# Kernel tuning notes

Hardware: AMD Instinct MI355X
Metric: run time of the kernel (lower is better)

## Reference

```python
import jax, jax.numpy as jnp
import numpy as np


def setup_inputs() -> dict:
    key = jax.random.key(0)
    k1, k2 = jax.random.split(key)
    B, S, D = 8, 4096, 1024
    E, P = 8, 4
    x = jax.random.normal(k1, (B, S, D), dtype=jnp.float32)
    phi_kernel = jax.random.normal(k2, (D, E * P), dtype=jnp.float32) * (1.0 / np.sqrt(D))
    phi_bias = jnp.zeros((E * P,), dtype=jnp.float32)
    return {"x": x, "phi_kernel": phi_kernel, "phi_bias": phi_bias,
            "num_experts": E, "num_slots": P}


def reference(x, phi_kernel, phi_bias, num_experts, num_slots):
    B, S, D = x.shape
    E, P = num_experts, num_slots
    # phi logits: [B,S,E,P]
    phi_logits = (jnp.einsum('bsd,dk->bsk', x, phi_kernel) + phi_bias).reshape(B, S, E, P)
    # softmax over the sequence axis (each slot is a convex combo of tokens)
    phi_weights = jax.nn.softmax(phi_logits, axis=1)
    # soft slots: weighted sum over tokens -> [B,E,P,D] (fused, no [B,S,E,P,D] blowup)
    soft_slots = jnp.einsum('bsd,bsep->bepd', x, phi_weights)
    expert_inputs = soft_slots.reshape(B, E, P * D)
    expert_weights = jnp.full((B, S, E), 1.0 / E, dtype=x.dtype)
    expert_indices = jnp.broadcast_to(jnp.arange(E, dtype=jnp.int32)[None, None, :], (B, S, E))
    return (expert_weights, expert_indices, phi_weights, soft_slots, expert_inputs)
```

## Files before the change

kernel.cpp:

```cpp
#include <hip/hip_runtime.h>
#include <hip/hip_bf16.h>

#define B 8
#define S 4096
#define DD 1024
#define KK 32

typedef __attribute__((ext_vector_type(8))) short bf16x8;
typedef __attribute__((ext_vector_type(16))) float f32x16;

static __device__ __forceinline__ unsigned short f2bf(float f) {
    unsigned int u = __builtin_bit_cast(unsigned int, f);
    u += 0x7FFFu + ((u >> 16) & 1u);
    return (unsigned short)(u >> 16);
}

__global__ __launch_bounds__(256) void k0_phit(const float* __restrict__ phi,
                                               unsigned short* __restrict__ phiT) {
    __shared__ float lt[32][33];
    const int d0 = blockIdx.x * 32;
    const int tid = threadIdx.x;
#pragma unroll
    for (int i = 0; i < 4; ++i) {
        int slot = tid + i * 256;
        int d = slot >> 5, k = slot & 31;
        lt[d][k] = phi[(size_t)(d0 + d) * KK + k];
    }
    __syncthreads();
    const int k = tid >> 3, c = tid & 7, d = c * 4;
    short4 pk;
    pk.x = (short)f2bf(lt[d + 0][k]);
    pk.y = (short)f2bf(lt[d + 1][k]);
    pk.z = (short)f2bf(lt[d + 2][k]);
    pk.w = (short)f2bf(lt[d + 3][k]);
    *(short4*)(phiT + (size_t)k * DD + d0 + d) = pk;
}

__global__ __launch_bounds__(256) void k1_logits(const float* __restrict__ x,
                                                 const unsigned short* __restrict__ phiT,
                                                 const float* __restrict__ bias,
                                                 float* __restrict__ lp) {
    __shared__ __align__(16) char sm[32768 + 2 * 16384];

    const int bid = blockIdx.x;
    const int dq = bid & 1;
    const int st = (bid >> 1) & 31;
    const int b  = bid >> 6;
    const int s0 = st * 128;
    const int tid = threadIdx.x;
    const int wv = __builtin_amdgcn_readfirstlane(tid >> 6);
    const int lane = tid & 63;
    const int l31 = lane & 31;
    const int half = lane >> 5;

    {
        const uint4* pg = (const uint4*)phiT;
#pragma unroll
        for (int i = 0; i < 8; ++i) {
            int slot = tid + i * 256;
            int k = slot >> 6, blk = slot & 63;
            uint4 v = pg[(size_t)k * 128 + dq * 64 + blk];
            *(uint4*)(sm + (size_t)k * 1024 + ((blk ^ (k & 7)) << 4)) = v;
        }
    }

    f32x16 acc;
    {
        float bv = (dq == 0) ? bias[l31] : 0.f;
#pragma unroll
        for (int r = 0; r < 16; ++r) acc[r] = bv;
    }

    const float* xg = x + ((size_t)(b * S + s0)) * DD + dq * 512;

    float4 q[8];
    auto load8 = [&](int ch) {
#pragma unroll
        for (int i = 0; i < 8; ++i) {
            int slot = tid + i * 256;
            int s = slot >> 4, c4 = slot & 15;
            q[i] = *(const float4*)(xg + (size_t)s * DD + ch * 64 + c4 * 4);
        }
    };
    auto store8 = [&](char* buf) {
#pragma unroll
        for (int i = 0; i < 8; ++i) {
            int slot = tid + i * 256;
            int s = slot >> 4, c4 = slot & 15;
            short4 pk;
            pk.x = (short)f2bf(q[i].x);
            pk.y = (short)f2bf(q[i].y);
            pk.z = (short)f2bf(q[i].z);
            pk.w = (short)f2bf(q[i].w);
            *(short4*)(buf + (size_t)s * 128 + (((c4 >> 1) ^ (s & 7)) << 4) + (c4 & 1) * 8) = pk;
        }
    };

    load8(0);
    store8(sm + 32768);
    __syncthreads();

    const int srow = wv * 32 + l31;
    const int sx = srow & 7;
    const int kx = l31 & 7;

    for (int ch = 0; ch < 8; ++ch) {
        char* cur = sm + 32768 + (ch & 1) * 16384;
        char* nxt = sm + 32768 + ((ch & 1) ^ 1) * 16384;
        if (ch < 7) load8(ch + 1);
#pragma unroll
        for (int step = 0; step < 4; ++step) {
            int blk = step * 2 + half;
            bf16x8 af  = *(const bf16x8*)(cur + (size_t)srow * 128 + ((blk ^ sx) << 4));
            bf16x8 bfv = *(const bf16x8*)(sm + (size_t)l31 * 1024 + (((ch * 8 + blk) ^ kx) << 4));
            acc = __builtin_amdgcn_mfma_f32_32x32x16_bf16(af, bfv, acc, 0, 0, 0);
        }
        __syncthreads();
        if (ch < 7) store8(nxt);
        __syncthreads();
    }

    float* lt = (float*)(sm + 32768);
#pragma unroll
    for (int r = 0; r < 16; ++r) {
        int row = (r & 3) + 8 * (r >> 2) + 4 * half;
        lt[(size_t)l31 * 129 + wv * 32 + row] = acc[r];
    }
    __syncthreads();
    float* o = lp + ((size_t)(dq * B + b) * KK) * S + s0;
#pragma unroll
    for (int i = 0; i < 4; ++i) {
        int slot = tid + i * 256;
        int k = slot >> 5, s4 = slot & 31;
        float4 v;
        v.x = lt[k * 129 + s4 * 4 + 0];
        v.y = lt[k * 129 + s4 * 4 + 1];
        v.z = lt[k * 129 + s4 * 4 + 2];
        v.w = lt[k * 129 + s4 * 4 + 3];
        *(float4*)(o + (size_t)k * S + s4 * 4) = v;
    }
}

__global__ __launch_bounds__(256) void k2a_partial(const float* __restrict__ lp,
                                                   float* __restrict__ pmax,
                                                   float* __restrict__ psum) {
    const int bid = blockIdx.x;
    const int c  = bid & 7;
    const int bk = bid >> 3;
    const int tid = threadIdx.x;
    const int wave = tid >> 6, lane = tid & 63;
    const size_t base = (size_t)bk * S + c * 512;

    float v0 = lp[base + tid]       + lp[1048576 + base + tid];
    float v1 = lp[base + tid + 256] + lp[1048576 + base + tid + 256];

    float m = fmaxf(v0, v1);
#pragma unroll
    for (int off = 32; off >= 1; off >>= 1) m = fmaxf(m, __shfl_xor(m, off, 64));
    __shared__ float sm_[4], sl[4];
    if (lane == 0) sm_[wave] = m;
    __syncthreads();
    const float M = fmaxf(fmaxf(sm_[0], sm_[1]), fmaxf(sm_[2], sm_[3]));

    float l = __expf(v0 - M) + __expf(v1 - M);
#pragma unroll
    for (int off = 32; off >= 1; off >>= 1) l += __shfl_xor(l, off, 64);
    if (lane == 0) sl[wave] = l;
    __syncthreads();
    if (tid == 0) {
        pmax[bid] = M;
        psum[bid] = sl[0] + sl[1] + sl[2] + sl[3];
    }
}

__global__ __launch_bounds__(256) void k2c_norm(const float* __restrict__ lp,
                                                const float* __restrict__ pmax,
                                                const float* __restrict__ psum,
                                                unsigned short* __restrict__ wbT,
                                                float* __restrict__ pw_out) {
    __shared__ float tile[128][33];
    __shared__ float sM[32], sLinv[32];
    const int b  = blockIdx.x >> 5;
    const int sc = blockIdx.x & 31;
    const int s0 = sc * 128;
    const int tid = threadIdx.x;

    if (tid < 32) {
        const int k = tid;
        float M = -1e30f, L = 0.f;
#pragma unroll
        for (int c = 0; c < 8; ++c) {
            float mc = pmax[(b * KK + k) * 8 + c];
            float lc = psum[(b * KK + k) * 8 + c];
            float nM = fmaxf(M, mc);
            L = L * __expf(M - nM) + lc * __expf(mc - nM);
            M = nM;
        }
        sM[k] = M;
        sLinv[k] = 1.0f / L;
    }
    __syncthreads();

    const int sL = tid & 127;
    const int kh = tid >> 7;
#pragma unroll
    for (int kk = 0; kk < 16; ++kk) {
        const int k = kk * 2 + kh;
        const size_t idx = ((size_t)b * KK + k) * S + s0 + sL;
        float v = lp[idx] + lp[1048576 + idx];
        float w = __expf(v - sM[k]) * sLinv[k];
        wbT[idx] = f2bf(w);
        tile[sL][k] = w;
    }
    __syncthreads();

    float* ob = pw_out + ((size_t)b * S + s0) * KK;
#pragma unroll
    for (int i = 0; i < 4; ++i) {
        const int idx4 = tid + i * 256;
        const int sl = idx4 >> 3, kq = idx4 & 7;
        float4 v4 = make_float4(tile[sl][kq * 4 + 0], tile[sl][kq * 4 + 1],
                                tile[sl][kq * 4 + 2], tile[sl][kq * 4 + 3]);
        ((float4*)ob)[idx4] = v4;
    }
}

__global__ __launch_bounds__(256) void k3_slots(const float* __restrict__ x,
                                                const unsigned int* __restrict__ wbT32,
                                                float* __restrict__ part) {
    __shared__ __align__(16) char sm[2 * 16384 + 2 * 4096];

    const int bid = blockIdx.x;
    const int sc = bid & 7;
    const int dg = (bid >> 3) & 7;
    const int b  = bid >> 6;
    const int tid = threadIdx.x;
    const int wv = __builtin_amdgcn_readfirstlane(tid >> 6);
    const int lane = tid & 63;
    const int l31 = lane & 31;
    const int half = lane >> 5;

    const int dth = tid & 127;
    const int sh  = tid >> 7;

    const float* xg = x + ((size_t)(b * S + sc * 512)) * DD + dg * 128 + dth;
    const unsigned int* wg = wbT32 + (size_t)b * KK * (S / 2) + sc * 256;

    float q0[16], q1[16];
    unsigned int qw[4];
    auto loadc = [&](int ch) {
#pragma unroll
        for (int j = 0; j < 16; ++j) {
            int sp = sh * 16 + j;
            q0[j] = xg[(size_t)(ch * 64 + sp * 2) * DD];
            q1[j] = xg[(size_t)(ch * 64 + sp * 2 + 1) * DD];
        }
#pragma unroll
        for (int i = 0; i < 4; ++i) {
            int slot = tid + i * 256;
            int k = slot >> 5, c = slot & 31;
            qw[i] = wg[(size_t)k * (S / 2) + ch * 32 + c];
        }
    };
    auto storec = [&](char* xB, char* wB) {
#pragma unroll
        for (int j = 0; j < 16; ++j) {
            int sp = sh * 16 + j;
            unsigned int pkd = (unsigned int)f2bf(q0[j]) | ((unsigned int)f2bf(q1[j]) << 16);
            *(unsigned int*)(xB + (size_t)dth * 128 + (((sp >> 2) ^ (dth & 7)) << 4) + (sp & 3) * 4) = pkd;
        }
#pragma unroll
        for (int i = 0; i < 4; ++i) {
            int slot = tid + i * 256;
            int k = slot >> 5, c = slot & 31;
            *(unsigned int*)(wB + (size_t)k * 128 + (((c >> 2) ^ (k & 7)) << 4) + (c & 3) * 4) = qw[i];
        }
    };

    f32x16 acc;
#pragma unroll
    for (int r = 0; r < 16; ++r) acc[r] = 0.f;

    loadc(0);
    storec(sm, sm + 32768);
    __syncthreads();

    const int dloc = wv * 32 + l31;
    const int dx = dloc & 7;
    const int kx = l31 & 7;

    for (int ch = 0; ch < 8; ++ch) {
        const int cur = ch & 1;
        char* xCur = sm + cur * 16384;
        char* wCur = sm + 32768 + cur * 4096;
        char* xNxt = sm + (cur ^ 1) * 16384;
        char* wNxt = sm + 32768 + (cur ^ 1) * 4096;
        if (ch < 7) loadc(ch + 1);
#pragma unroll
        for (int step = 0; step < 4; ++step) {
            int blk = step * 2 + half;
            bf16x8 af  = *(const bf16x8*)(wCur + (size_t)l31 * 128 + ((blk ^ kx) << 4));
            bf16x8 bfv = *(const bf16x8*)(xCur + (size_t)dloc * 128 + ((blk ^ dx) << 4));
            acc = __builtin_amdgcn_mfma_f32_32x32x16_bf16(af, bfv, acc, 0, 0, 0);
        }
        __syncthreads();
        if (ch < 7) storec(xNxt, wNxt);
        __syncthreads();
    }

    float* pp = part + (((size_t)sc * B + b) * KK) * DD + dg * 128 + wv * 32 + l31;
#pragma unroll
    for (int r = 0; r < 16; ++r) {
        int k = (r & 3) + 8 * (r >> 2) + 4 * half;
        pp[(size_t)k * DD] = acc[r];
    }
}

__global__ __launch_bounds__(256) void k4_finalize(const float* __restrict__ part,
                                                   float* __restrict__ out) {
    const int idx = blockIdx.x * 256 + threadIdx.x;
    const float4* p4 = (const float4*)part;

    float4 sv = p4[idx];
#pragma unroll
    for (int c = 1; c < 8; ++c) {
        float4 t = p4[(size_t)c * 65536 + idx];
        sv.x += t.x; sv.y += t.y; sv.z += t.z; sv.w += t.w;
    }

    ((float4*)(out + 1572864))[idx] = sv;
    ((float4*)(out + 1835008))[idx] = sv;
    ((float4*)out)[idx] = make_float4(0.125f, 0.125f, 0.125f, 0.125f);
    float base = (float)((idx * 4) & 7);
    ((float4*)(out + 262144))[idx] = make_float4(base, base + 1.f, base + 2.f, base + 3.f);
}

extern "C" void kernel_launch(void* const* d_in, const int* in_sizes, int n_in,
                              void* d_out, int out_size, void* d_ws, size_t ws_size,
                              hipStream_t stream) {
    const float* x    = (const float*)d_in[0];
    const float* phi  = (const float*)d_in[1];
    const float* bias = (const float*)d_in[2];
    float* out = (float*)d_out;

    float* ws = (float*)d_ws;
    float* lp   = ws;
    float* pmax = ws + 2097152;
    float* psum = ws + 2099200;
    unsigned short* wbT  = (unsigned short*)(ws + 2101248);
    unsigned short* phiT = (unsigned short*)(ws + 2625536);
    float* part = ws + 2641920;
    float* pw_out = out + 524288;

    k0_phit<<<dim3(32), dim3(256), 0, stream>>>(phi, phiT);
    k1_logits<<<dim3(512), dim3(256), 0, stream>>>(x, phiT, bias, lp);
    k2a_partial<<<dim3(2048), dim3(256), 0, stream>>>(lp, pmax, psum);
    k2c_norm<<<dim3(256), dim3(256), 0, stream>>>(lp, pmax, psum, wbT, pw_out);
    k3_slots<<<dim3(512), dim3(256), 0, stream>>>(x, (const unsigned int*)wbT, part);
    k4_finalize<<<dim3(256), dim3(256), 0, stream>>>(part, out);
}
```

Before: 234.6 us.

## Load MFMA operands directly from global in logits and use async LDS loads in slots

```diff
diff --git a/kernel.cpp b/kernel.cpp
--- a/kernel.cpp
+++ b/kernel.cpp
@@ -13,6 +13,16 @@
     unsigned int u = __builtin_bit_cast(unsigned int, f);
     u += 0x7FFFu + ((u >> 16) & 1u);
     return (unsigned short)(u >> 16);
+}
+
+static __device__ __forceinline__ unsigned int pack2bf(float lo, float hi) {
+    return (unsigned int)f2bf(lo) | ((unsigned int)f2bf(hi) << 16);
+}
+
+static __device__ __forceinline__ void gload_lds16(const void* g, void* l) {
+    __builtin_amdgcn_global_load_lds(
+        (const __attribute__((address_space(1))) unsigned int*)g,
+        (__attribute__((address_space(3))) unsigned int*)l, 16, 0, 0);
 }
 
 __global__ __launch_bounds__(256) void k0_phit(const float* __restrict__ phi,
@@ -40,13 +50,13 @@
                                                  const unsigned short* __restrict__ phiT,
                                                  const float* __restrict__ bias,
                                                  float* __restrict__ lp) {
-    __shared__ __align__(16) char sm[32768 + 2 * 16384];
+    __shared__ __align__(16) char sm[32768];
+    __shared__ float lt[32][129];
 
     const int bid = blockIdx.x;
     const int dq = bid & 1;
     const int st = (bid >> 1) & 31;
     const int b  = bid >> 6;
-    const int s0 = st * 128;
     const int tid = threadIdx.x;
     const int wv = __builtin_amdgcn_readfirstlane(tid >> 6);
     const int lane = tid & 63;
@@ -70,73 +80,43 @@
 #pragma unroll
         for (int r = 0; r < 16; ++r) acc[r] = bv;
     }
-
-    const float* xg = x + ((size_t)(b * S + s0)) * DD + dq * 512;
-
-    float4 q[8];
-    auto load8 = [&](int ch) {
-#pragma unroll
-        for (int i = 0; i < 8; ++i) {
-            int slot = tid + i * 256;
-            int s = slot >> 4, c4 = slot & 15;
-            q[i] = *(const float4*)(xg + (size_t)s * DD + ch * 64 + c4 * 4);
-        }
-    };
-    auto store8 = [&](char* buf) {
-#pragma unroll
-        for (int i = 0; i < 8; ++i) {
-            int slot = tid + i * 256;
-            int s = slot >> 4, c4 = slot & 15;
-            short4 pk;
-            pk.x = (short)f2bf(q[i].x);
-            pk.y = (short)f2bf(q[i].y);
-            pk.z = (short)f2bf(q[i].z);
-            pk.w = (short)f2bf(q[i].w);
-            *(short4*)(buf + (size_t)s * 128 + (((c4 >> 1) ^ (s & 7)) << 4) + (c4 & 1) * 8) = pk;
-        }
-    };
-
-    load8(0);
-    store8(sm + 32768);
-    __syncthreads();
-
-    const int srow = wv * 32 + l31;
-    const int sx = srow & 7;
+    __syncthreads();
+
+    const float* xg = x + ((size_t)(b * S + st * 128 + wv * 32 + l31)) * DD
+                        + dq * 512 + half * 8;
     const int kx = l31 & 7;
-
-    for (int ch = 0; ch < 8; ++ch) {
-        char* cur = sm + 32768 + (ch & 1) * 16384;
-        char* nxt = sm + 32768 + ((ch & 1) ^ 1) * 16384;
-        if (ch < 7) load8(ch + 1);
-#pragma unroll
-        for (int step = 0; step < 4; ++step) {
-            int blk = step * 2 + half;
-            bf16x8 af  = *(const bf16x8*)(cur + (size_t)srow * 128 + ((blk ^ sx) << 4));
-            bf16x8 bfv = *(const bf16x8*)(sm + (size_t)l31 * 1024 + (((ch * 8 + blk) ^ kx) << 4));
-            acc = __builtin_amdgcn_mfma_f32_32x32x16_bf16(af, bfv, acc, 0, 0, 0);
-        }
-        __syncthreads();
-        if (ch < 7) store8(nxt);
-        __syncthreads();
-    }
-
-    float* lt = (float*)(sm + 32768);
+    const char* brow = sm + (size_t)l31 * 1024;
+
+#pragma unroll 8
+    for (int ch = 0; ch < 32; ++ch) {
+        float4 a0 = *(const float4*)(xg + ch * 16);
+        float4 a1 = *(const float4*)(xg + ch * 16 + 4);
+        unsigned int p0 = pack2bf(a0.x, a0.y);
+        unsigned int p1 = pack2bf(a0.z, a0.w);
+        unsigned int p2 = pack2bf(a1.x, a1.y);
+        unsigned int p3 = pack2bf(a1.z, a1.w);
+        uint4 pv = make_uint4(p0, p1, p2, p3);
+        bf16x8 af = __builtin_bit_cast(bf16x8, pv);
+        bf16x8 bfv = *(const bf16x8*)(brow + (((ch * 2 + half) ^ kx) << 4));
+        acc = __builtin_amdgcn_mfma_f32_32x32x16_bf16(af, bfv, acc, 0, 0, 0);
+    }
+
 #pragma unroll
     for (int r = 0; r < 16; ++r) {
         int row = (r & 3) + 8 * (r >> 2) + 4 * half;
-        lt[(size_t)l31 * 129 + wv * 32 + row] = acc[r];
-    }
-    __syncthreads();
-    float* o = lp + ((size_t)(dq * B + b) * KK) * S + s0;
+        lt[l31][wv * 32 + row] = acc[r];
+    }
+    __syncthreads();
+    float* o = lp + ((size_t)(dq * B + b) * KK) * S + st * 128;
 #pragma unroll
     for (int i = 0; i < 4; ++i) {
         int slot = tid + i * 256;
         int k = slot >> 5, s4 = slot & 31;
         float4 v;
-        v.x = lt[k * 129 + s4 * 4 + 0];
-        v.y = lt[k * 129 + s4 * 4 + 1];
-        v.z = lt[k * 129 + s4 * 4 + 2];
-        v.w = lt[k * 129 + s4 * 4 + 3];
+        v.x = lt[k][s4 * 4 + 0];
+        v.y = lt[k][s4 * 4 + 1];
+        v.z = lt[k][s4 * 4 + 2];
+        v.w = lt[k][s4 * 4 + 3];
         *(float4*)(o + (size_t)k * S + s4 * 4) = v;
     }
 }
@@ -226,9 +206,9 @@
 }
 
 __global__ __launch_bounds__(256) void k3_slots(const float* __restrict__ x,
-                                                const unsigned int* __restrict__ wbT32,
+                                                const unsigned short* __restrict__ wbT,
                                                 float* __restrict__ part) {
-    __shared__ __align__(16) char sm[2 * 16384 + 2 * 4096];
+    __shared__ __align__(16) char sm[2 * 32768 + 2 * 4096];
 
     const int bid = blockIdx.x;
     const int sc = bid & 7;
@@ -240,75 +220,55 @@
     const int l31 = lane & 31;
     const int half = lane >> 5;
 
-    const int dth = tid & 127;
-    const int sh  = tid >> 7;
-
-    const float* xg = x + ((size_t)(b * S + sc * 512)) * DD + dg * 128 + dth;
-    const unsigned int* wg = wbT32 + (size_t)b * KK * (S / 2) + sc * 256;
-
-    float q0[16], q1[16];
-    unsigned int qw[4];
-    auto loadc = [&](int ch) {
-#pragma unroll
-        for (int j = 0; j < 16; ++j) {
-            int sp = sh * 16 + j;
-            q0[j] = xg[(size_t)(ch * 64 + sp * 2) * DD];
-            q1[j] = xg[(size_t)(ch * 64 + sp * 2 + 1) * DD];
-        }
-#pragma unroll
-        for (int i = 0; i < 4; ++i) {
-            int slot = tid + i * 256;
-            int k = slot >> 5, c = slot & 31;
-            qw[i] = wg[(size_t)k * (S / 2) + ch * 32 + c];
-        }
+    const char* xsrc = (const char*)(x + ((size_t)(b * S + sc * 512 + wv * 16 + half)) * DD
+                                       + dg * 128 + l31 * 4);
+    const int wk = wv * 8 + (lane >> 3);
+    const char* wsrc = (const char*)wbT + ((size_t)(b * KK + wk) * S + sc * 512) * 2
+                                        + (((lane & 7) ^ (wk & 7)) << 4);
+
+    char* const xb0 = sm;
+    char* const wb0 = sm + 65536;
+
+    auto stage = [&](int ch, int buf) {
+        char* xb = xb0 + buf * 32768 + wv * (16 * 512);
+        const char* xs = xsrc + (size_t)ch * (64 * DD * 4);
+#pragma unroll
+        for (int t = 0; t < 8; ++t)
+            gload_lds16(xs + (size_t)t * (2 * DD * 4), xb + t * 1024);
+        gload_lds16(wsrc + (size_t)ch * 128, wb0 + buf * 4096 + wv * 1024);
     };
-    auto storec = [&](char* xB, char* wB) {
-#pragma unroll
-        for (int j = 0; j < 16; ++j) {
-            int sp = sh * 16 + j;
-            unsigned int pkd = (unsigned int)f2bf(q0[j]) | ((unsigned int)f2bf(q1[j]) << 16);
-            *(unsigned int*)(xB + (size_t)dth * 128 + (((sp >> 2) ^ (dth & 7)) << 4) + (sp & 3) * 4) = pkd;
-        }
-#pragma unroll
-        for (int i = 0; i < 4; ++i) {
-            int slot = tid + i * 256;
-            int k = slot >> 5, c = slot & 31;
-            *(unsigned int*)(wB + (size_t)k * 128 + (((c >> 2) ^ (k & 7)) << 4) + (c & 3) * 4) = qw[i];
-        }
-    };
 
     f32x16 acc;
 #pragma unroll
     for (int r = 0; r < 16; ++r) acc[r] = 0.f;
 
-    loadc(0);
-    storec(sm, sm + 32768);
-    __syncthreads();
-
-    const int dloc = wv * 32 + l31;
-    const int dx = dloc & 7;
+    stage(0, 0);
+    __syncthreads();
+
+    const int col = wv * 32 + l31;
     const int kx = l31 & 7;
 
     for (int ch = 0; ch < 8; ++ch) {
         const int cur = ch & 1;
-        char* xCur = sm + cur * 16384;
-        char* wCur = sm + 32768 + cur * 4096;
-        char* xNxt = sm + (cur ^ 1) * 16384;
-        char* wNxt = sm + 32768 + (cur ^ 1) * 4096;
-        if (ch < 7) loadc(ch + 1);
+        if (ch < 7) stage(ch + 1, cur ^ 1);
+        const float* xr = (const float*)(xb0 + cur * 32768);
+        const char* wr = wb0 + cur * 4096 + (size_t)l31 * 128;
 #pragma unroll
         for (int step = 0; step < 4; ++step) {
-            int blk = step * 2 + half;
-            bf16x8 af  = *(const bf16x8*)(wCur + (size_t)l31 * 128 + ((blk ^ kx) << 4));
-            bf16x8 bfv = *(const bf16x8*)(xCur + (size_t)dloc * 128 + ((blk ^ dx) << 4));
+            bf16x8 af = *(const bf16x8*)(wr + (((step * 2 + half) ^ kx) << 4));
+            const int sb = step * 16 + half * 8;
+            unsigned int p0 = pack2bf(xr[(sb + 0) * 128 + col], xr[(sb + 1) * 128 + col]);
+            unsigned int p1 = pack2bf(xr[(sb + 2) * 128 + col], xr[(sb + 3) * 128 + col]);
+            unsigned int p2 = pack2bf(xr[(sb + 4) * 128 + col], xr[(sb + 5) * 128 + col]);
+            unsigned int p3 = pack2bf(xr[(sb + 6) * 128 + col], xr[(sb + 7) * 128 + col]);
+            uint4 pv = make_uint4(p0, p1, p2, p3);
+            bf16x8 bfv = __builtin_bit_cast(bf16x8, pv);
             acc = __builtin_amdgcn_mfma_f32_32x32x16_bf16(af, bfv, acc, 0, 0, 0);
         }
         __syncthreads();
-        if (ch < 7) storec(xNxt, wNxt);
-        __syncthreads();
-    }
-
-    float* pp = part + (((size_t)sc * B + b) * KK) * DD + dg * 128 + wv * 32 + l31;
+    }
+
+    float* pp = part + (((size_t)sc * B + b) * KK) * DD + dg * 128 + col;
 #pragma unroll
     for (int r = 0; r < 16; ++r) {
         int k = (r & 3) + 8 * (r >> 2) + 4 * half;
@@ -356,6 +316,6 @@
     k1_logits<<<dim3(512), dim3(256), 0, stream>>>(x, phiT, bias, lp);
     k2a_partial<<<dim3(2048), dim3(256), 0, stream>>>(lp, pmax, psum);
     k2c_norm<<<dim3(256), dim3(256), 0, stream>>>(lp, pmax, psum, wbT, pw_out);
-    k3_slots<<<dim3(512), dim3(256), 0, stream>>>(x, (const unsigned int*)wbT, part);
+    k3_slots<<<dim3(512), dim3(256), 0, stream>>>(x, wbT, part);
     k4_finalize<<<dim3(256), dim3(256), 0, stream>>>(part, out);
 }
```

Measured after the change: 237.1 us. About the same (+1.1%).
